# Performance work log

Hardware: AMD Instinct MI355X
Metric: run time of the kernel (lower is better)

## Reference

```python
import jax, jax.numpy as jnp
import numpy as np

EMBED = 128
HEADS = 32
HEAD_DIM = EMBED // HEADS  # 4
BATCH = 32
SEQ = 2048


def setup_inputs() -> dict:
    key = jax.random.key(0)
    ks = jax.random.split(key, 6)
    s = 1.0 / np.sqrt(EMBED)
    return {
        "x": jax.random.normal(ks[0], (BATCH, SEQ, EMBED), dtype=jnp.float32),
        # torch Linear weights are (out_features, in_features)
        "Wq": jax.random.uniform(ks[1], (EMBED, EMBED), jnp.float32, -s, s),
        "Wk": jax.random.uniform(ks[2], (EMBED, EMBED), jnp.float32, -s, s),
        "Wv": jax.random.uniform(ks[3], (EMBED, EMBED), jnp.float32, -s, s),
        "Wo": jax.random.uniform(ks[4], (EMBED, EMBED), jnp.float32, -s, s),
        "bo": jax.random.uniform(ks[5], (EMBED,), jnp.float32, -s, s),
    }


def reference(x, Wq, Wk, Wv, Wo, bo):
    b, s, e = x.shape
    h, d = HEADS, HEAD_DIM
    # projections (torch Linear: x @ W.T)
    q = (x @ Wq.T).reshape(b, s, h, d)
    k = (x @ Wk.T).reshape(b, s, h, d)
    v = (x @ Wv.T).reshape(b, s, h, d)
    # FAITHFUL to source: einsum 'bnqh,bnkh->bnqk' on (b, seq, heads, head_dim)
    # => n = seq position, q/k = HEADS. Attention is over the heads axis.
    scale = 1.0 / (float(d) ** 0.5)
    scores = jnp.einsum('bnqh,bnkh->bnqk', q, k) * scale  # (b, seq, heads, heads)
    attn = jax.nn.softmax(scores, axis=-1)
    attended = jnp.einsum('bnqk,bnkv->bnqv', attn, v).reshape(b, s, e)
    return attended @ Wo.T + bo
```

## Files before the change

kernel.cpp:

```cpp
#include <hip/hip_runtime.h>


#define TOKENS (32 * 2048)
#define E 128
#define NH 32
#define WTOK 16
#define THREADS 128
#define LPITCH 136

typedef __attribute__((ext_vector_type(4))) float f32x4;
typedef __attribute__((ext_vector_type(16))) float f32x16;
typedef __fp16 h8_t __attribute__((ext_vector_type(8)));

#if __has_builtin(__builtin_amdgcn_exp2f)
#define EXP2F __builtin_amdgcn_exp2f
#else
#define EXP2F exp2f
#endif

#if __has_builtin(__builtin_amdgcn_rcpf)
#define RCPF __builtin_amdgcn_rcpf
#else
#define RCPF(x) (1.0f / (x))
#endif

static __device__ __forceinline__ unsigned pk16(float a, float b) {
    return __builtin_bit_cast(unsigned, __builtin_amdgcn_cvt_pkrtz(a, b));
}

static __device__ __forceinline__ f32x16 zero16() {
    f32x16 z;
#pragma unroll
    for (int i = 0; i < 16; ++i) z[i] = 0.f;
    return z;
}

static __device__ __forceinline__ int vperm(int kh) {
    return ((kh >> 4) & 1) * 16 + ((kh >> 2) & 1) * 8 + ((kh >> 3) & 1) * 4 + (kh & 3);
}

__global__ void pack_w(const float* __restrict__ Wq, const float* __restrict__ Wk,
                       const float* __restrict__ Wv, const float* __restrict__ Wo,
                       __fp16* __restrict__ wpk) {
    int idx = blockIdx.x * blockDim.x + threadIdx.x;
    if (idx >= 4 * 8 * 4 * 64) return;
    int lane = idx & 63;
    int ks   = (idx >> 6) & 3;
    int nt   = (idx >> 8) & 7;
    int proj = idx >> 11;
    const float* W = (proj == 0) ? Wq : (proj == 1) ? Wk : (proj == 2) ? Wv : Wo;
    float scl = (proj == 1) ? 0.72134752044448170f : 1.0f;
    int c = lane & 15, g = lane >> 4;
    const float* src = W + (size_t)(nt * 16 + c) * E + ks * 32 + g * 8;
    __fp16* dst = wpk + (size_t)idx * 8;
#pragma unroll
    for (int j = 0; j < 8; ++j) dst[j] = (__fp16)(src[j] * scl);
}

__global__ __launch_bounds__(THREADS) void mha_fused(
        const float* __restrict__ x, const __fp16* __restrict__ wpk,
        const float* __restrict__ bo, float* __restrict__ out) {
    __shared__ __align__(16) __fp16 qs [2 * WTOK * LPITCH];
    __shared__ __align__(16) __fp16 ksh[2 * WTOK * LPITCH];
    __shared__ __align__(16) __fp16 vth[2 * WTOK * LPITCH];

    const int tid  = threadIdx.x;
    const int wave = tid >> 6;
    const int lane = tid & 63;
    const int c = lane & 15, g = lane >> 4;
    const int tbase = blockIdx.x * (2 * WTOK) + wave * WTOK;

    __fp16* qsw = qs  + wave * WTOK * LPITCH;
    __fp16* ksw = ksh + wave * WTOK * LPITCH;
    __fp16* vtw = vth + wave * WTOK * LPITCH;

    {
        h8_t afrag[4];
        const float* xrow = x + (size_t)(tbase + c) * E;
#pragma unroll
        for (int ks2 = 0; ks2 < 4; ++ks2) {
            const float* p = xrow + ks2 * 32 + g * 8;
            float4 v0 = *(const float4*)(p);
            float4 v1 = *(const float4*)(p + 4);
            uint4 au;
            au.x = pk16(v0.x, v0.y);
            au.y = pk16(v0.z, v0.w);
            au.z = pk16(v1.x, v1.y);
            au.w = pk16(v1.z, v1.w);
            afrag[ks2] = __builtin_bit_cast(h8_t, au);
        }

        h8_t wfb[3][4];
#pragma unroll
        for (int p = 0; p < 3; ++p) {
            const __fp16* wb = wpk + ((size_t)(p * 4) * 64 + lane) * 8;
#pragma unroll
            for (int k = 0; k < 4; ++k)
                wfb[p][k] = *(const h8_t*)(wb + (size_t)k * 64 * 8);
        }

#pragma unroll
        for (int nc = 0; nc < 24; ++nc) {
            const int proj = nc >> 3;
            const int nt   = nc & 7;
            const int slot = nc % 3;
            f32x4 acc = {0.f, 0.f, 0.f, 0.f};
#pragma unroll
            for (int ks2 = 0; ks2 < 4; ++ks2) {
                acc = __builtin_amdgcn_mfma_f32_16x16x32_f16(wfb[slot][ks2], afrag[ks2], acc, 0, 0, 0);
            }
            if (nc + 3 < 24) {
                const __fp16* wb = wpk + ((size_t)((nc + 3) * 4) * 64 + lane) * 8;
#pragma unroll
                for (int k = 0; k < 4; ++k)
                    wfb[slot][k] = *(const h8_t*)(wb + (size_t)k * 64 * 8);
            }
            if (proj < 2) {
                __fp16* dst = proj ? ksw : qsw;
                uint2 st = make_uint2(pk16(acc[0], acc[1]), pk16(acc[2], acc[3]));
                *(uint2*)(dst + c * LPITCH + nt * 16 + g * 4) = st;
            } else {
                int vp = vperm(nt * 4 + g);
#pragma unroll
                for (int r2 = 0; r2 < 4; ++r2)
                    vtw[c * LPITCH + r2 * 32 + vp] = (__fp16)acc[r2];
            }
        }
    }

    {
        const int c32 = lane & 31;
        const int gg  = lane >> 5;
        const uint4 ONES4 = make_uint4(0x3C003C00u, 0x3C003C00u, 0x3C003C00u, 0x3C003C00u);
        const f32x16 z = zero16();

        uint4 ka0[2], qa0[2], ka1[2], qa1[2];
        uint4 va00[2], va01[2], va10[2], va11[2];

#define LOADPAIR(s, pr_) do {                                                  \
        const int t0_ = (pr_) * 2, t1_ = t0_ + 1;                              \
        ka0[s] = qa0[s] = ka1[s] = qa1[s] = make_uint4(0u, 0u, 0u, 0u);        \
        if (gg == 0) {                                                         \
            uint2 t_;                                                          \
            t_ = *(const uint2*)(ksw + t0_ * LPITCH + c32 * 4); ka0[s].x = t_.x; ka0[s].y = t_.y; \
            t_ = *(const uint2*)(qsw + t0_ * LPITCH + c32 * 4); qa0[s].x = t_.x; qa0[s].y = t_.y; \
            t_ = *(const uint2*)(ksw + t1_ * LPITCH + c32 * 4); ka1[s].x = t_.x; ka1[s].y = t_.y; \
            t_ = *(const uint2*)(qsw + t1_ * LPITCH + c32 * 4); qa1[s].x = t_.x; qa1[s].y = t_.y; \
        }                                                                      \
        va00[s] = *(const uint4*)(vtw + t0_ * LPITCH + (c32 & 3) * 32 + gg * 8);      \
        va01[s] = *(const uint4*)(vtw + t0_ * LPITCH + (c32 & 3) * 32 + 16 + gg * 8); \
        va10[s] = *(const uint4*)(vtw + t1_ * LPITCH + (c32 & 3) * 32 + gg * 8);      \
        va11[s] = *(const uint4*)(vtw + t1_ * LPITCH + (c32 & 3) * 32 + 16 + gg * 8); \
        if (c32 == 4) { va00[s] = ONES4; va01[s] = ONES4; va10[s] = ONES4; va11[s] = ONES4; } \
    } while (0)

        LOADPAIR(0, 0);
#pragma unroll
        for (int pr = 0; pr < 8; ++pr) {
            const int s = pr & 1;
            if (pr < 7) LOADPAIR(s ^ 1, pr + 1);

            const int t0 = pr * 2, t1 = t0 + 1;

            f32x16 sc0 = __builtin_amdgcn_mfma_f32_32x32x16_f16(
                __builtin_bit_cast(h8_t, ka0[s]), __builtin_bit_cast(h8_t, qa0[s]), z, 0, 0, 0);
            f32x16 sc1 = __builtin_amdgcn_mfma_f32_32x32x16_f16(
                __builtin_bit_cast(h8_t, ka1[s]), __builtin_bit_cast(h8_t, qa1[s]), z, 0, 0, 0);

            uint4 p00u, p01u, p10u, p11u;
            {
                float e[16];
#pragma unroll
                for (int r = 0; r < 16; ++r) e[r] = EXP2F(sc0[r]);
                p00u = make_uint4(pk16(e[0], e[1]),  pk16(e[2], e[3]),
                                  pk16(e[4], e[5]),  pk16(e[6], e[7]));
                p01u = make_uint4(pk16(e[8], e[9]),  pk16(e[10], e[11]),
                                  pk16(e[12], e[13]), pk16(e[14], e[15]));
            }
            {
                float e[16];
#pragma unroll
                for (int r = 0; r < 16; ++r) e[r] = EXP2F(sc1[r]);
                p10u = make_uint4(pk16(e[0], e[1]),  pk16(e[2], e[3]),
                                  pk16(e[4], e[5]),  pk16(e[6], e[7]));
                p11u = make_uint4(pk16(e[8], e[9]),  pk16(e[10], e[11]),
                                  pk16(e[12], e[13]), pk16(e[14], e[15]));
            }

            f32x16 pv0 = __builtin_amdgcn_mfma_f32_32x32x16_f16(
                __builtin_bit_cast(h8_t, va00[s]), __builtin_bit_cast(h8_t, p00u), z, 0, 0, 0);
            pv0 = __builtin_amdgcn_mfma_f32_32x32x16_f16(
                __builtin_bit_cast(h8_t, va01[s]), __builtin_bit_cast(h8_t, p01u), pv0, 0, 0, 0);
            f32x16 pv1 = __builtin_amdgcn_mfma_f32_32x32x16_f16(
                __builtin_bit_cast(h8_t, va10[s]), __builtin_bit_cast(h8_t, p10u), z, 0, 0, 0);
            pv1 = __builtin_amdgcn_mfma_f32_32x32x16_f16(
                __builtin_bit_cast(h8_t, va11[s]), __builtin_bit_cast(h8_t, p11u), pv1, 0, 0, 0);

            float s0 = __shfl(pv0[0], c32 + 32, 64);
            float s1 = __shfl(pv1[0], c32 + 32, 64);
            float r0 = RCPF(s0), r1 = RCPF(s1);
            if (lane < 32) {
                uint2 st0 = make_uint2(pk16(pv0[0] * r0, pv0[1] * r0),
                                       pk16(pv0[2] * r0, pv0[3] * r0));
                uint2 st1 = make_uint2(pk16(pv1[0] * r1, pv1[1] * r1),
                                       pk16(pv1[2] * r1, pv1[3] * r1));
                *(uint2*)(qsw + t0 * LPITCH + c32 * 4) = st0;
                *(uint2*)(qsw + t1 * LPITCH + c32 * 4) = st1;
            }
        }
#undef LOADPAIR
    }

    {
        h8_t af[4];
#pragma unroll
        for (int ks2 = 0; ks2 < 4; ++ks2)
            af[ks2] = *(const h8_t*)(qsw + c * LPITCH + ks2 * 32 + g * 8);

        h8_t wob[3][4];
#pragma unroll
        for (int p = 0; p < 3; ++p) {
            const __fp16* wb = wpk + ((size_t)((3 * 8 + p) * 4) * 64 + lane) * 8;
#pragma unroll
            for (int k = 0; k < 4; ++k)
                wob[p][k] = *(const h8_t*)(wb + (size_t)k * 64 * 8);
        }

#pragma unroll
        for (int nt = 0; nt < 8; ++nt) {
            const int slot = nt % 3;
            f32x4 acc = {0.f, 0.f, 0.f, 0.f};
#pragma unroll
            for (int ks2 = 0; ks2 < 4; ++ks2)
                acc = __builtin_amdgcn_mfma_f32_16x16x32_f16(wob[slot][ks2], af[ks2], acc, 0, 0, 0);
            if (nt + 3 < 8) {
                const __fp16* wb = wpk + ((size_t)((3 * 8 + nt + 3) * 4) * 64 + lane) * 8;
#pragma unroll
                for (int k = 0; k < 4; ++k)
                    wob[slot][k] = *(const h8_t*)(wb + (size_t)k * 64 * 8);
            }
            int col0 = nt * 16 + g * 4;
            float4 b4 = *(const float4*)(bo + col0);
            float4 st = make_float4(acc[0] + b4.x, acc[1] + b4.y,
                                    acc[2] + b4.z, acc[3] + b4.w);
            *(float4*)(out + (size_t)(tbase + c) * E + col0) = st;
        }
    }
}

extern "C" void kernel_launch(void* const* d_in, const int* in_sizes, int n_in,
                              void* d_out, int out_size, void* d_ws, size_t ws_size,
                              hipStream_t stream) {
    const float* x  = (const float*)d_in[0];
    const float* Wq = (const float*)d_in[1];
    const float* Wk = (const float*)d_in[2];
    const float* Wv = (const float*)d_in[3];
    const float* Wo = (const float*)d_in[4];
    const float* bo = (const float*)d_in[5];
    __fp16* wpk = (__fp16*)d_ws;
    float* out = (float*)d_out;

    pack_w<<<32, 256, 0, stream>>>(Wq, Wk, Wv, Wo, wpk);
    mha_fused<<<TOKENS / (2 * WTOK), THREADS, 0, stream>>>(x, wpk, bo, out);
}
```

Before: 41.53 us.

## Halve tokens per wave to double grid size and drop weight prefetch ring

```diff
diff --git a/kernel.cpp b/kernel.cpp
--- a/kernel.cpp
+++ b/kernel.cpp
@@ -4,7 +4,7 @@
 #define TOKENS (32 * 2048)
 #define E 128
 #define NH 32
-#define WTOK 16
+#define WTOK 8
 #define THREADS 128
 #define LPITCH 136
 
@@ -68,6 +68,7 @@
     const int wave = tid >> 6;
     const int lane = tid & 63;
     const int c = lane & 15, g = lane >> 4;
+    const int tc = c & 7;
     const int tbase = blockIdx.x * (2 * WTOK) + wave * WTOK;
 
     __fp16* qsw = qs  + wave * WTOK * LPITCH;
@@ -76,7 +77,7 @@
 
     {
         h8_t afrag[4];
-        const float* xrow = x + (size_t)(tbase + c) * E;
+        const float* xrow = x + (size_t)(tbase + tc) * E;
 #pragma unroll
         for (int ks2 = 0; ks2 < 4; ++ks2) {
             const float* p = xrow + ks2 * 32 + g * 8;
@@ -90,40 +91,28 @@
             afrag[ks2] = __builtin_bit_cast(h8_t, au);
         }
 
-        h8_t wfb[3][4];
-#pragma unroll
-        for (int p = 0; p < 3; ++p) {
-            const __fp16* wb = wpk + ((size_t)(p * 4) * 64 + lane) * 8;
-#pragma unroll
-            for (int k = 0; k < 4; ++k)
-                wfb[p][k] = *(const h8_t*)(wb + (size_t)k * 64 * 8);
-        }
-
 #pragma unroll
         for (int nc = 0; nc < 24; ++nc) {
             const int proj = nc >> 3;
             const int nt   = nc & 7;
-            const int slot = nc % 3;
+            const __fp16* wb = wpk + ((size_t)(nc * 4) * 64 + lane) * 8;
             f32x4 acc = {0.f, 0.f, 0.f, 0.f};
 #pragma unroll
             for (int ks2 = 0; ks2 < 4; ++ks2) {
-                acc = __builtin_amdgcn_mfma_f32_16x16x32_f16(wfb[slot][ks2], afrag[ks2], acc, 0, 0, 0);
-            }
-            if (nc + 3 < 24) {
-                const __fp16* wb = wpk + ((size_t)((nc + 3) * 4) * 64 + lane) * 8;
-#pragma unroll
-                for (int k = 0; k < 4; ++k)
-                    wfb[slot][k] = *(const h8_t*)(wb + (size_t)k * 64 * 8);
-            }
-            if (proj < 2) {
-                __fp16* dst = proj ? ksw : qsw;
-                uint2 st = make_uint2(pk16(acc[0], acc[1]), pk16(acc[2], acc[3]));
-                *(uint2*)(dst + c * LPITCH + nt * 16 + g * 4) = st;
-            } else {
-                int vp = vperm(nt * 4 + g);
-#pragma unroll
-                for (int r2 = 0; r2 < 4; ++r2)
-                    vtw[c * LPITCH + r2 * 32 + vp] = (__fp16)acc[r2];
+                h8_t wf = *(const h8_t*)(wb + (size_t)ks2 * 64 * 8);
+                acc = __builtin_amdgcn_mfma_f32_16x16x32_f16(wf, afrag[ks2], acc, 0, 0, 0);
+            }
+            if (c < 8) {
+                if (proj < 2) {
+                    __fp16* dst = proj ? ksw : qsw;
+                    uint2 st = make_uint2(pk16(acc[0], acc[1]), pk16(acc[2], acc[3]));
+                    *(uint2*)(dst + c * LPITCH + nt * 16 + g * 4) = st;
+                } else {
+                    int vp = vperm(nt * 4 + g);
+#pragma unroll
+                    for (int r2 = 0; r2 < 4; ++r2)
+                        vtw[c * LPITCH + r2 * 32 + vp] = (__fp16)acc[r2];
+                }
             }
         }
     }
@@ -156,9 +145,9 @@
 
         LOADPAIR(0, 0);
 #pragma unroll
-        for (int pr = 0; pr < 8; ++pr) {
+        for (int pr = 0; pr < 4; ++pr) {
             const int s = pr & 1;
-            if (pr < 7) LOADPAIR(s ^ 1, pr + 1);
+            if (pr < 3) LOADPAIR(s ^ 1, pr + 1);
 
             const int t0 = pr * 2, t1 = t0 + 1;
 
@@ -215,35 +204,24 @@
         h8_t af[4];
 #pragma unroll
         for (int ks2 = 0; ks2 < 4; ++ks2)
-            af[ks2] = *(const h8_t*)(qsw + c * LPITCH + ks2 * 32 + g * 8);
-
-        h8_t wob[3][4];
-#pragma unroll
-        for (int p = 0; p < 3; ++p) {
-            const __fp16* wb = wpk + ((size_t)((3 * 8 + p) * 4) * 64 + lane) * 8;
-#pragma unroll
-            for (int k = 0; k < 4; ++k)
-                wob[p][k] = *(const h8_t*)(wb + (size_t)k * 64 * 8);
-        }
+            af[ks2] = *(const h8_t*)(qsw + tc * LPITCH + ks2 * 32 + g * 8);
 
 #pragma unroll
         for (int nt = 0; nt < 8; ++nt) {
-            const int slot = nt % 3;
+            const __fp16* wb = wpk + ((size_t)((3 * 8 + nt) * 4) * 64 + lane) * 8;
             f32x4 acc = {0.f, 0.f, 0.f, 0.f};
 #pragma unroll
-            for (int ks2 = 0; ks2 < 4; ++ks2)
-                acc = __builtin_amdgcn_mfma_f32_16x16x32_f16(wob[slot][ks2], af[ks2], acc, 0, 0, 0);
-            if (nt + 3 < 8) {
-                const __fp16* wb = wpk + ((size_t)((3 * 8 + nt + 3) * 4) * 64 + lane) * 8;
-#pragma unroll
-                for (int k = 0; k < 4; ++k)
-                    wob[slot][k] = *(const h8_t*)(wb + (size_t)k * 64 * 8);
-            }
-            int col0 = nt * 16 + g * 4;
-            float4 b4 = *(const float4*)(bo + col0);
-            float4 st = make_float4(acc[0] + b4.x, acc[1] + b4.y,
-                                    acc[2] + b4.z, acc[3] + b4.w);
-            *(float4*)(out + (size_t)(tbase + c) * E + col0) = st;
+            for (int ks2 = 0; ks2 < 4; ++ks2) {
+                h8_t b = *(const h8_t*)(wb + (size_t)ks2 * 64 * 8);
+                acc = __builtin_amdgcn_mfma_f32_16x16x32_f16(b, af[ks2], acc, 0, 0, 0);
+            }
+            if (c < 8) {
+                int col0 = nt * 16 + g * 4;
+                float4 b4 = *(const float4*)(bo + col0);
+                float4 st = make_float4(acc[0] + b4.x, acc[1] + b4.y,
+                                        acc[2] + b4.z, acc[3] + b4.w);
+                *(float4*)(out + (size_t)(tbase + c) * E + col0) = st;
+            }
         }
     }
 }
```

Result: slower. 68.16 us (+64.1%).
